# Kernel optimization log

Measured on AMD Instinct MI355X. Metric: run time of the kernel, lower is better.

The kernel has to match this reference:

```python
import jax, jax.numpy as jnp
import numpy as np

N = 50000
E = 800000
F_IN = 128
HID = 16
HEADS = 8
CLS = 16
NEG_SLOPE = 0.2


def setup_inputs() -> dict:
    key = jax.random.key(0)
    ks = jax.random.split(key, 12)
    x = jax.random.normal(ks[0], (N, F_IN), dtype=jnp.float32)
    edge_index = jax.random.randint(ks[1], (2, E), 0, N, dtype=jnp.int32)
    s = 0.1
    W1 = jax.random.normal(ks[2], (F_IN, HEADS * HID), dtype=jnp.float32) * s
    att_src1 = jax.random.normal(ks[3], (HEADS, HID), dtype=jnp.float32) * s
    att_dst1 = jax.random.normal(ks[4], (HEADS, HID), dtype=jnp.float32) * s
    b1 = jax.random.normal(ks[5], (HEADS * HID,), dtype=jnp.float32) * s
    W2 = jax.random.normal(ks[6], (HEADS * HID, CLS), dtype=jnp.float32) * s
    att_src2 = jax.random.normal(ks[7], (1, CLS), dtype=jnp.float32) * s
    att_dst2 = jax.random.normal(ks[8], (1, CLS), dtype=jnp.float32) * s
    b2 = jax.random.normal(ks[9], (CLS,), dtype=jnp.float32) * s
    return {"x": x, "edge_index": edge_index, "W1": W1, "att_src1": att_src1,
            "att_dst1": att_dst1, "b1": b1, "W2": W2, "att_src2": att_src2,
            "att_dst2": att_dst2, "b2": b2}


def _gat_conv(x, src, dst, W, a_src, a_dst, b, heads, out_ch, concat):
    n = x.shape[0]
    h = (x @ W).reshape(n, heads, out_ch)                     # [N,H,C]
    alpha_src = (h * a_src[None]).sum(-1)                     # [N,H]
    alpha_dst = (h * a_dst[None]).sum(-1)                     # [N,H]
    e = jax.nn.leaky_relu(alpha_src[src] + alpha_dst[dst], NEG_SLOPE)  # [E,H]
    m = jax.lax.stop_gradient(jax.ops.segment_max(e, dst, num_segments=n))
    e = jnp.exp(e - m[dst])
    denom = jax.ops.segment_sum(e, dst, num_segments=n)
    alpha = e / (denom[dst] + 1e-16)                          # [E,H]
    msg = h[src] * alpha[:, :, None]                          # [E,H,C]
    out = jax.ops.segment_sum(msg, dst, num_segments=n)       # [N,H,C]
    out = out.reshape(n, heads * out_ch) if concat else out.mean(axis=1)
    return out + b


def reference(x, edge_index, W1, att_src1, att_dst1, b1, W2, att_src2, att_dst2, b2):
    # PyG GATConv default add_self_loops=True
    loop = jnp.arange(N, dtype=edge_index.dtype)
    src = jnp.concatenate([edge_index[0], loop])
    dst = jnp.concatenate([edge_index[1], loop])
    h = _gat_conv(x, src, dst, W1, att_src1, att_dst1, b1, HEADS, HID, True)
    h = jax.nn.elu(h)
    # dropout inactive (eval mode)
    out = _gat_conv(h, src, dst, W2, att_src2, att_dst2, b2, 1, CLS, False)
    return out
```

## Files before the change

kernel.cpp:

```cpp
#include <hip/hip_runtime.h>
#include <hip/hip_bf16.h>
#include <limits.h>
#include <math.h>

#define N 50000
#define E_ 800000
#define ETOT 850000
#define HH 128
#define HEADS 8
#define HID 16
#define CLS 16
#define NEG 0.2f
#define NB ((N + 255) / 256)
#define GBM 64
#define GEMM_NB ((N + GBM - 1) / GBM)
#define LINK_NB ((ETOT + 255) / 256)
#define A1_NB ((N*HEADS + 255) / 256)

typedef unsigned short u16;
typedef unsigned int   u32;
typedef short s8v __attribute__((ext_vector_type(8)));
typedef float f4v __attribute__((ext_vector_type(4)));

__device__ __forceinline__ u16 f2bu(float f){
  union{float f; u32 i;} c; c.f = f;
  u32 lsb = (c.i >> 16) & 1u;
  c.i += 0x7fffu + lsb;
  return (u16)(c.i >> 16);
}
__device__ __forceinline__ float bu2f(u16 u){
  union{u32 i; float f;} c; c.i = ((u32)u) << 16; return c.f;
}
__device__ __forceinline__ float blo(u32 u){ union{u32 i; float f;} c; c.i = u << 16; return c.f; }
__device__ __forceinline__ float bhi(u32 u){ union{u32 i; float f;} c; c.i = u & 0xffff0000u; return c.f; }

__global__ __launch_bounds__(256) void k_prepW(const float* __restrict__ W,
                                               u16* __restrict__ wth, u16* __restrict__ wtl){
  int i = blockIdx.x*256 + threadIdx.x;
  if(i >= 128*128) return;
  int k = i >> 7, c = i & 127;
  float v = W[i];
  u16 hi = f2bu(v);
  u16 lo = f2bu(v - bu2f(hi));
  wth[c*128 + k] = hi;
  wtl[c*128 + k] = lo;
}

__global__ __launch_bounds__(256) void k_gemm1link(const float* __restrict__ x,
                                                   const u16* __restrict__ wth,
                                                   const u16* __restrict__ wtl,
                                                   u16* __restrict__ h1b,
                                                   const int* __restrict__ ei,
                                                   int* __restrict__ head,
                                                   int* __restrict__ srcv,
                                                   int* __restrict__ nxt){
  __shared__ u16 xh[GBM][40], xl[GBM][40];
  __shared__ u16 wh[128][40], wl[128][40];
  if(blockIdx.x >= GEMM_NB){
    int e = (blockIdx.x - GEMM_NB)*256 + threadIdx.x;
    if(e < ETOT){
      int s, d;
      if(e < E_){ s = ei[e]; d = ei[E_ + e]; } else { s = d = e - E_; }
      int old = atomicExch(&head[d], e);
      srcv[e] = s;
      nxt[e]  = old;
    }
    return;
  }
  int tid  = threadIdx.x;
  int wv   = tid >> 6;
  int lane = tid & 63;
  int row0 = blockIdx.x * GBM;

  f4v acc[4][2];
  #pragma unroll
  for(int t=0;t<4;t++)
    #pragma unroll
    for(int u=0;u<2;u++) acc[t][u] = (f4v){0.f,0.f,0.f,0.f};

  int xr  = tid >> 2;
  int xkq = (tid & 3) * 8;
  int wc  = tid & 127;
  int wq  = (tid >> 7) * 8;
  int xrow = row0 + xr; if(xrow >= N) xrow = N-1;
  const float* xb = x + (size_t)xrow*128 + xkq;
  int fr = lane & 15, fg = lane >> 4;
  int kk = fg*8;

  for(int kc=0; kc<4; kc++){
    int k0 = kc*32;
    float4 v0 = *(const float4*)(xb + k0);
    float4 v1 = *(const float4*)(xb + k0 + 4);
    __syncthreads();
    {
      float vv[8] = {v0.x,v0.y,v0.z,v0.w,v1.x,v1.y,v1.z,v1.w};
      s8v H, L;
      #pragma unroll
      for(int j=0;j<8;j++){
        u16 h_ = f2bu(vv[j]);
        H[j] = (short)h_;
        L[j] = (short)f2bu(vv[j] - bu2f(h_));
      }
      *(s8v*)&xh[xr][xkq] = H;
      *(s8v*)&xl[xr][xkq] = L;
    }
    #pragma unroll
    for(int j=0;j<2;j++){
      int kq = wq + j*16;
      *(s8v*)&wh[wc][kq] = *(const s8v*)&wth[wc*128 + k0 + kq];
      *(s8v*)&wl[wc][kq] = *(const s8v*)&wtl[wc*128 + k0 + kq];
    }
    __syncthreads();
    s8v a_h[4], a_l[4], b_h[2], b_l[2];
    #pragma unroll
    for(int t=0;t<4;t++){
      a_h[t] = *(const s8v*)&xh[t*16 + fr][kk];
      a_l[t] = *(const s8v*)&xl[t*16 + fr][kk];
    }
    #pragma unroll
    for(int u=0;u<2;u++){
      int col = wv*32 + u*16 + fr;
      b_h[u] = *(const s8v*)&wh[col][kk];
      b_l[u] = *(const s8v*)&wl[col][kk];
    }
    #pragma unroll
    for(int t=0;t<4;t++){
      #pragma unroll
      for(int u=0;u<2;u++){
        acc[t][u] = __builtin_amdgcn_mfma_f32_16x16x32_bf16(a_h[t], b_h[u], acc[t][u], 0,0,0);
        acc[t][u] = __builtin_amdgcn_mfma_f32_16x16x32_bf16(a_h[t], b_l[u], acc[t][u], 0,0,0);
        acc[t][u] = __builtin_amdgcn_mfma_f32_16x16x32_bf16(a_l[t], b_h[u], acc[t][u], 0,0,0);
      }
    }
  }
  #pragma unroll
  for(int t=0;t<4;t++){
    #pragma unroll
    for(int j=0;j<4;j++){
      int row = row0 + t*16 + fg*4 + j;
      if(row < N){
        u16* dst = h1b + (size_t)row*128 + wv*32 + fr;
        dst[0]  = f2bu(acc[t][0][j]);
        dst[16] = f2bu(acc[t][1][j]);
      }
    }
  }
}

__global__ __launch_bounds__(256) void k_alphascan1(const u16* __restrict__ h1b,
                                                    const float* __restrict__ Asv,
                                                    const float* __restrict__ Adv,
                                                    float* __restrict__ as1,
                                                    float* __restrict__ ad1,
                                                    const int* __restrict__ head,
                                                    const int* __restrict__ nxt,
                                                    int* __restrict__ deg,
                                                    int* __restrict__ bsum){
  __shared__ int sm[256];
  if(blockIdx.x < NB){
    int t = threadIdx.x;
    int i = blockIdx.x*256 + t;
    int cnt = 0;
    if(i < N){
      int e = head[i];
      while(e >= 0){ cnt++; e = nxt[e]; }
      deg[i] = cnt;
    }
    sm[t] = cnt;
    __syncthreads();
    #pragma unroll
    for(int ofs=128; ofs>0; ofs>>=1){
      if(t < ofs) sm[t] += sm[t+ofs];
      __syncthreads();
    }
    if(t == 0) bsum[blockIdx.x] = sm[0];
    return;
  }
  int id = (blockIdx.x - NB)*256 + threadIdx.x;
  if(id >= N*HEADS) return;
  int i = id >> 3, h = id & 7;
  const uint4* hv = (const uint4*)(h1b + (size_t)i*HH + h*HID);
  uint4 u0 = hv[0], u1 = hv[1];
  float vals[16] = {blo(u0.x),bhi(u0.x),blo(u0.y),bhi(u0.y),
                    blo(u0.z),bhi(u0.z),blo(u0.w),bhi(u0.w),
                    blo(u1.x),bhi(u1.x),blo(u1.y),bhi(u1.y),
                    blo(u1.z),bhi(u1.z),blo(u1.w),bhi(u1.w)};
  float s=0.f, d=0.f;
  #pragma unroll
  for(int j=0;j<16;j++){
    s = fmaf(vals[j], Asv[h*HID+j], s);
    d = fmaf(vals[j], Adv[h*HID+j], d);
  }
  as1[id]=s; ad1[id]=d;
}

__global__ __launch_bounds__(256) void k_scan3walk(const int* __restrict__ deg,
                                                   const int* __restrict__ bsum,
                                                   const int* __restrict__ head,
                                                   const int* __restrict__ srcv,
                                                   const int* __restrict__ nxt,
                                                   int* __restrict__ off,
                                                   int* __restrict__ csr){
  __shared__ int red[256];
  __shared__ int sm[256];
  int t = threadIdx.x;
  red[t] = (t < blockIdx.x) ? bsum[t] : 0;
  __syncthreads();
  #pragma unroll
  for(int ofs=128; ofs>0; ofs>>=1){
    if(t < ofs) red[t] += red[t+ofs];
    __syncthreads();
  }
  int boff = red[0];
  int i = blockIdx.x*256 + t;
  int v0 = (i < N) ? deg[i] : 0;
  sm[t] = v0;
  __syncthreads();
  #pragma unroll
  for(int ofs=1; ofs<256; ofs<<=1){
    int v = sm[t];
    int add = (t >= ofs) ? sm[t-ofs] : 0;
    __syncthreads();
    sm[t] = v + add;
    __syncthreads();
  }
  if(i < N){
    int excl = boff + sm[t] - v0;
    off[i] = excl;
    if(i == N-1) off[N] = excl + v0;
    int e = head[i];
    int pos = excl;
    while(e >= 0){
      csr[pos++] = srcv[e];
      e = nxt[e];
    }
  }
}

#define CH 64
__global__ __launch_bounds__(256) void k_agg1(const int* __restrict__ off,
                                              const int* __restrict__ csr,
                                              const float* __restrict__ as1,
                                              const float* __restrict__ ad1,
                                              const u32* __restrict__ h1w,
                                              const float* __restrict__ b1,
                                              u32* __restrict__ helu_w){
  __shared__ float wsm[4][CH*8];
  __shared__ int   ssm[4][CH];
  int wv   = threadIdx.x >> 6;
  int lane = threadIdx.x & 63;
  int node = blockIdx.x*4 + wv;
  int beg = off[node], end = off[node+1];
  int h  = lane >> 3;
  int hh = lane & 7;
  int el = lane >> 3;
  float advA = ad1[node*8 + hh];
  float den = 0.f, num0 = 0.f, num1 = 0.f;
  float* wsw = wsm[wv];
  int*   ssw = ssm[wv];
  const u32* hp = h1w + lane;
  for(int base = beg; base < end; base += CH){
    int cnt = end - base; if(cnt > CH) cnt = CH;
    #pragma unroll
    for(int k=0;k<CH;k+=8){
      int e = el + k;
      if(e < cnt){
        int s = csr[base+e];
        if(hh == 0) ssw[e] = s;
        float v = as1[s*8+hh] + advA;
        v = v > 0.f ? v : NEG*v;
        wsw[e*8+hh] = __expf(v);
      }
    }
    int e = 0;
    for(; e+8 <= cnt; e += 8){
      int ss[8]; float ww[8]; u32 uu[8];
      #pragma unroll
      for(int j=0;j<8;j++){ ss[j] = ssw[e+j]; ww[j] = wsw[(e+j)*8+h]; }
      #pragma unroll
      for(int j=0;j<8;j++){ uu[j] = hp[(size_t)ss[j]*64]; }
      #pragma unroll
      for(int j=0;j<8;j++){
        den += ww[j];
        num0 = fmaf(ww[j], blo(uu[j]), num0);
        num1 = fmaf(ww[j], bhi(uu[j]), num1);
      }
    }
    for(; e < cnt; e++){
      int s = ssw[e];
      float w = wsw[e*8+h];
      u32 u = hp[(size_t)s*64];
      den += w;
      num0 = fmaf(w, blo(u), num0);
      num1 = fmaf(w, bhi(u), num1);
    }
  }
  float2 bb = ((const float2*)b1)[lane];
  float inv = 1.f / (den + 1e-16f);
  float r0 = num0*inv + bb.x;
  float r1 = num1*inv + bb.y;
  r0 = r0 > 0.f ? r0 : expm1f(r0);
  r1 = r1 > 0.f ? r1 : expm1f(r1);
  helu_w[(size_t)node*64 + lane] = (u32)f2bu(r0) | ((u32)f2bu(r1) << 16);
}

__global__ __launch_bounds__(256) void k_gemm2(const u16* __restrict__ hb,
                                               const float* __restrict__ W2,
                                               const float* __restrict__ Asv,
                                               const float* __restrict__ Adv,
                                               u16* __restrict__ h2b,
                                               float* __restrict__ as2,
                                               float* __restrict__ ad2){
  __shared__ float Wl[128*16];
  int tid = threadIdx.x;
  const float4* W4 = (const float4*)W2;
  float4* Wl4 = (float4*)Wl;
  Wl4[tid]       = W4[tid];
  Wl4[tid + 256] = W4[tid + 256];
  __syncthreads();
  int i = blockIdx.x*16 + (tid >> 4);
  int c = tid & 15;
  if(i >= N) return;
  const uint4* h8 = (const uint4*)(hb + (size_t)i*HH);
  float acc = 0.f;
  #pragma unroll
  for(int ch=0; ch<16; ch++){
    uint4 u = h8[ch];
    int k = ch*8;
    acc = fmaf(blo(u.x), Wl[(k+0)*16+c], acc);
    acc = fmaf(bhi(u.x), Wl[(k+1)*16+c], acc);
    acc = fmaf(blo(u.y), Wl[(k+2)*16+c], acc);
    acc = fmaf(bhi(u.y), Wl[(k+3)*16+c], acc);
    acc = fmaf(blo(u.z), Wl[(k+4)*16+c], acc);
    acc = fmaf(bhi(u.z), Wl[(k+5)*16+c], acc);
    acc = fmaf(blo(u.w), Wl[(k+6)*16+c], acc);
    acc = fmaf(bhi(u.w), Wl[(k+7)*16+c], acc);
  }
  h2b[(size_t)i*CLS + c] = f2bu(acc);
  float ps = acc * Asv[c];
  float pd = acc * Adv[c];
  ps += __shfl_xor(ps,1); ps += __shfl_xor(ps,2); ps += __shfl_xor(ps,4); ps += __shfl_xor(ps,8);
  pd += __shfl_xor(pd,1); pd += __shfl_xor(pd,2); pd += __shfl_xor(pd,4); pd += __shfl_xor(pd,8);
  if(c == 0){ as2[i] = ps; ad2[i] = pd; }
}

__global__ __launch_bounds__(256) void k_agg2(const int* __restrict__ off,
                                              const int* __restrict__ csr,
                                              const float* __restrict__ as2,
                                              const float* __restrict__ ad2,
                                              const u32* __restrict__ h2w,
                                              const float* __restrict__ b2,
                                              float* __restrict__ outp){
  int t = threadIdx.x;
  int node = blockIdx.x*32 + (t >> 3);
  int c2 = t & 7;
  if(node >= N) return;
  int beg = off[node], end = off[node+1];
  float adv = ad2[node];
  float den = 0.f, num0 = 0.f, num1 = 0.f;
  for(int base = beg; base < end; base += 8){
    int cnt = end - base; if(cnt > 8) cnt = 8;
    float w_my = 0.f; int s_my = 0;
    if(c2 < cnt){
      s_my = csr[base + c2];
      float v = as2[s_my] + adv;
      v = v > 0.f ? v : NEG*v;
      w_my = __expf(v);
    }
    #pragma unroll
    for(int j=0; j<8; j++){
      if(j >= cnt) break;
      int src = (t & 56) | j;
      float w = __shfl(w_my, src);
      int   s = __shfl(s_my, src);
      u32 u = h2w[(size_t)s*8 + c2];
      den += w;
      num0 = fmaf(w, blo(u), num0);
      num1 = fmaf(w, bhi(u), num1);
    }
  }
  float inv = 1.f / (den + 1e-16f);
  float2 bb = ((const float2*)b2)[c2];
  float2 r;
  r.x = num0*inv + bb.x;
  r.y = num1*inv + bb.y;
  ((float2*)outp)[(size_t)node*8 + c2] = r;
}

extern "C" void kernel_launch(void* const* d_in, const int* in_sizes, int n_in,
                              void* d_out, int out_size, void* d_ws, size_t ws_size,
                              hipStream_t stream){
  const float* x     = (const float*)d_in[0];
  const int*   ei    = (const int*)  d_in[1];
  const float* W1    = (const float*)d_in[2];
  const float* av_s1 = (const float*)d_in[3];
  const float* av_d1 = (const float*)d_in[4];
  const float* b1    = (const float*)d_in[5];
  const float* W2    = (const float*)d_in[6];
  const float* av_s2 = (const float*)d_in[7];
  const float* av_d2 = (const float*)d_in[8];
  const float* b2    = (const float*)d_in[9];
  float* outp = (float*)d_out;

  char* p = (char*)d_ws;
  auto alloc = [&](size_t bytes){ char* q = p; p += (bytes + 255) & ~(size_t)255; return q; };
  u16*   h1b    = (u16*)  alloc((size_t)N*HH*2);
  u16*   helu_b = (u16*)  alloc((size_t)N*HH*2);
  u16*   h2b    = (u16*)  alloc((size_t)N*CLS*2);
  float* as1    = (float*)alloc((size_t)N*HEADS*4);
  float* ad1    = (float*)alloc((size_t)N*HEADS*4);
  float* as2    = (float*)alloc((size_t)N*4);
  float* ad2    = (float*)alloc((size_t)N*4);
  int*   deg    = (int*)  alloc((size_t)N*4);
  int*   head   = (int*)  alloc((size_t)N*4);
  int*   off    = (int*)  alloc((size_t)(N+1)*4);
  int*   csr    = (int*)  alloc((size_t)ETOT*4);
  int*   srcv   = (int*)  alloc((size_t)ETOT*4);
  int*   nxt    = (int*)  alloc((size_t)ETOT*4);
  u16*   wth    = (u16*)  alloc((size_t)128*128*2);
  u16*   wtl    = (u16*)  alloc((size_t)128*128*2);
  int*   bsum   = (int*)  alloc((size_t)NB*4);

  hipMemsetAsync(head, 0xFF, (size_t)N*4, stream);

  k_prepW<<<(128*128+255)/256, 256, 0, stream>>>(W1, wth, wtl);

  k_gemm1link<<<GEMM_NB + LINK_NB, 256, 0, stream>>>(x, wth, wtl, h1b, ei, head, srcv, nxt);

  k_alphascan1<<<NB + A1_NB, 256, 0, stream>>>(h1b, av_s1, av_d1, as1, ad1, head, nxt, deg, bsum);

  k_scan3walk<<<NB, 256, 0, stream>>>(deg, bsum, head, srcv, nxt, off, csr);

  k_agg1<<<N/4, 256, 0, stream>>>(off, csr, as1, ad1, (const u32*)h1b, b1, (u32*)helu_b);

  k_gemm2<<<(N+15)/16, 256, 0, stream>>>(helu_b, W2, av_s2, av_d2, h2b, as2, ad2);
  k_agg2<<<(N+31)/32, 256, 0, stream>>>(off, csr, as2, ad2, (const u32*)h2b, b2, outp);
}
```

Before: 160.4 us.

## Use MFMA for layer-2 GEMM, batch gathers in aggregation kernels, shrink agg1 chunk

Replaces the scalar FMA layer-2 GEMM with a bf16 MFMA kernel that uses split hi/lo W2 weights prepared alongside W1 in a merged prep kernel. Separately, agg1's edge chunk shrinks from 64 to 32 and gains a 4-wide unrolled gather tail, and agg2's gather loop is restructured to issue all 8 loads before accumulating. The aim is more memory-level parallelism in the gathers and less ALU time in gemm2, at the cost of extra workspace and a bf16 split approximation of W2.

```diff
diff --git a/kernel.cpp b/kernel.cpp
--- a/kernel.cpp
+++ b/kernel.cpp
@@ -34,16 +34,25 @@
 __device__ __forceinline__ float blo(u32 u){ union{u32 i; float f;} c; c.i = u << 16; return c.f; }
 __device__ __forceinline__ float bhi(u32 u){ union{u32 i; float f;} c; c.i = u & 0xffff0000u; return c.f; }
 
-__global__ __launch_bounds__(256) void k_prepW(const float* __restrict__ W,
-                                               u16* __restrict__ wth, u16* __restrict__ wtl){
+__global__ __launch_bounds__(256) void k_prep(const float* __restrict__ W1,
+                                              const float* __restrict__ W2,
+                                              u16* __restrict__ wth, u16* __restrict__ wtl,
+                                              u16* __restrict__ w2th, u16* __restrict__ w2tl){
   int i = blockIdx.x*256 + threadIdx.x;
-  if(i >= 128*128) return;
-  int k = i >> 7, c = i & 127;
-  float v = W[i];
-  u16 hi = f2bu(v);
-  u16 lo = f2bu(v - bu2f(hi));
-  wth[c*128 + k] = hi;
-  wtl[c*128 + k] = lo;
+  if(i < 128*128){
+    int k = i >> 7, c = i & 127;
+    float v = W1[i];
+    u16 hi = f2bu(v);
+    wth[c*128 + k] = hi;
+    wtl[c*128 + k] = f2bu(v - bu2f(hi));
+  }
+  if(i < 128*16){
+    int k = i >> 4, c = i & 15;
+    float v = W2[i];
+    u16 hi = f2bu(v);
+    w2th[c*128 + k] = hi;
+    w2tl[c*128 + k] = f2bu(v - bu2f(hi));
+  }
 }
 
 __global__ __launch_bounds__(256) void k_gemm1link(const float* __restrict__ x,
@@ -237,7 +246,7 @@
   }
 }
 
-#define CH 64
+#define CH 32
 __global__ __launch_bounds__(256) void k_agg1(const int* __restrict__ off,
                                               const int* __restrict__ csr,
                                               const float* __restrict__ as1,
@@ -286,6 +295,19 @@
         num1 = fmaf(ww[j], bhi(uu[j]), num1);
       }
     }
+    for(; e+4 <= cnt; e += 4){
+      int ss[4]; float ww[4]; u32 uu[4];
+      #pragma unroll
+      for(int j=0;j<4;j++){ ss[j] = ssw[e+j]; ww[j] = wsw[(e+j)*8+h]; }
+      #pragma unroll
+      for(int j=0;j<4;j++){ uu[j] = hp[(size_t)ss[j]*64]; }
+      #pragma unroll
+      for(int j=0;j<4;j++){
+        den += ww[j];
+        num0 = fmaf(ww[j], blo(uu[j]), num0);
+        num1 = fmaf(ww[j], bhi(uu[j]), num1);
+      }
+    }
     for(; e < cnt; e++){
       int s = ssw[e];
       float w = wsw[e*8+h];
@@ -304,44 +326,57 @@
   helu_w[(size_t)node*64 + lane] = (u32)f2bu(r0) | ((u32)f2bu(r1) << 16);
 }
 
-__global__ __launch_bounds__(256) void k_gemm2(const u16* __restrict__ hb,
-                                               const float* __restrict__ W2,
-                                               const float* __restrict__ Asv,
-                                               const float* __restrict__ Adv,
-                                               u16* __restrict__ h2b,
-                                               float* __restrict__ as2,
-                                               float* __restrict__ ad2){
-  __shared__ float Wl[128*16];
-  int tid = threadIdx.x;
-  const float4* W4 = (const float4*)W2;
-  float4* Wl4 = (float4*)Wl;
-  Wl4[tid]       = W4[tid];
-  Wl4[tid + 256] = W4[tid + 256];
+__global__ __launch_bounds__(256) void k_gemm2m(const u16* __restrict__ helu,
+                                                const u16* __restrict__ w2th,
+                                                const u16* __restrict__ w2tl,
+                                                const float* __restrict__ Asv,
+                                                const float* __restrict__ Adv,
+                                                u16* __restrict__ h2b,
+                                                float* __restrict__ as2,
+                                                float* __restrict__ ad2){
+  __shared__ u16 At[4][16][136];
+  __shared__ u16 Bh[16][136], Bl[16][136];
+  int tid  = threadIdx.x;
+  int wv   = tid >> 6;
+  int lane = tid & 63;
+  int fr = lane & 15, fg = lane >> 4;
+  int row0 = blockIdx.x*64 + wv*16;
+
+  {
+    int r = tid >> 4, c8 = (tid & 15)*8;
+    *(s8v*)&Bh[r][c8] = *(const s8v*)&w2th[r*128 + c8];
+    *(s8v*)&Bl[r][c8] = *(const s8v*)&w2tl[r*128 + c8];
+  }
+  #pragma unroll
+  for(int j=0;j<4;j++){
+    int rl = j*4 + (lane >> 4);
+    int rg = row0 + rl; if(rg >= N) rg = N-1;
+    *(s8v*)&At[wv][rl][(lane & 15)*8] = *(const s8v*)&helu[(size_t)rg*128 + (lane & 15)*8];
+  }
   __syncthreads();
-  int i = blockIdx.x*16 + (tid >> 4);
-  int c = tid & 15;
-  if(i >= N) return;
-  const uint4* h8 = (const uint4*)(hb + (size_t)i*HH);
-  float acc = 0.f;
-  #pragma unroll
-  for(int ch=0; ch<16; ch++){
-    uint4 u = h8[ch];
-    int k = ch*8;
-    acc = fmaf(blo(u.x), Wl[(k+0)*16+c], acc);
-    acc = fmaf(bhi(u.x), Wl[(k+1)*16+c], acc);
-    acc = fmaf(blo(u.y), Wl[(k+2)*16+c], acc);
-    acc = fmaf(bhi(u.y), Wl[(k+3)*16+c], acc);
-    acc = fmaf(blo(u.z), Wl[(k+4)*16+c], acc);
-    acc = fmaf(bhi(u.z), Wl[(k+5)*16+c], acc);
-    acc = fmaf(blo(u.w), Wl[(k+6)*16+c], acc);
-    acc = fmaf(bhi(u.w), Wl[(k+7)*16+c], acc);
-  }
-  h2b[(size_t)i*CLS + c] = f2bu(acc);
-  float ps = acc * Asv[c];
-  float pd = acc * Adv[c];
-  ps += __shfl_xor(ps,1); ps += __shfl_xor(ps,2); ps += __shfl_xor(ps,4); ps += __shfl_xor(ps,8);
-  pd += __shfl_xor(pd,1); pd += __shfl_xor(pd,2); pd += __shfl_xor(pd,4); pd += __shfl_xor(pd,8);
-  if(c == 0){ as2[i] = ps; ad2[i] = pd; }
+
+  f4v acc = (f4v){0.f,0.f,0.f,0.f};
+  #pragma unroll
+  for(int kc=0; kc<4; kc++){
+    int kk = kc*32 + fg*8;
+    s8v a  = *(const s8v*)&At[wv][fr][kk];
+    s8v bh = *(const s8v*)&Bh[fr][kk];
+    s8v bl = *(const s8v*)&Bl[fr][kk];
+    acc = __builtin_amdgcn_mfma_f32_16x16x32_bf16(a, bh, acc, 0,0,0);
+    acc = __builtin_amdgcn_mfma_f32_16x16x32_bf16(a, bl, acc, 0,0,0);
+  }
+  float asv = Asv[fr], adv = Adv[fr];
+  #pragma unroll
+  for(int j=0;j<4;j++){
+    int row = row0 + fg*4 + j;
+    float ps = acc[j]*asv, pd = acc[j]*adv;
+    ps += __shfl_xor(ps,1); ps += __shfl_xor(ps,2); ps += __shfl_xor(ps,4); ps += __shfl_xor(ps,8);
+    pd += __shfl_xor(pd,1); pd += __shfl_xor(pd,2); pd += __shfl_xor(pd,4); pd += __shfl_xor(pd,8);
+    if(row < N){
+      h2b[(size_t)row*16 + fr] = f2bu(acc[j]);
+      if(fr == 0){ as2[row] = ps; ad2[row] = pd; }
+    }
+  }
 }
 
 __global__ __launch_bounds__(256) void k_agg2(const int* __restrict__ off,
@@ -358,6 +393,7 @@
   int beg = off[node], end = off[node+1];
   float adv = ad2[node];
   float den = 0.f, num0 = 0.f, num1 = 0.f;
+  int gbase = t & 56;
   for(int base = beg; base < end; base += 8){
     int cnt = end - base; if(cnt > 8) cnt = 8;
     float w_my = 0.f; int s_my = 0;
@@ -367,16 +403,23 @@
       v = v > 0.f ? v : NEG*v;
       w_my = __expf(v);
     }
-    #pragma unroll
-    for(int j=0; j<8; j++){
-      if(j >= cnt) break;
-      int src = (t & 56) | j;
-      float w = __shfl(w_my, src);
-      int   s = __shfl(s_my, src);
-      u32 u = h2w[(size_t)s*8 + c2];
-      den += w;
-      num0 = fmaf(w, blo(u), num0);
-      num1 = fmaf(w, bhi(u), num1);
+    float ww[8]; int ss[8]; u32 uu[8];
+    #pragma unroll
+    for(int j=0;j<8;j++){
+      ww[j] = __shfl(w_my, gbase | j);
+      ss[j] = __shfl(s_my, gbase | j);
+    }
+    #pragma unroll
+    for(int j=0;j<8;j++){
+      if(j < cnt) uu[j] = h2w[(size_t)ss[j]*8 + c2];
+    }
+    #pragma unroll
+    for(int j=0;j<8;j++){
+      if(j < cnt){
+        den += ww[j];
+        num0 = fmaf(ww[j], blo(uu[j]), num0);
+        num1 = fmaf(ww[j], bhi(uu[j]), num1);
+      }
     }
   }
   float inv = 1.f / (den + 1e-16f);
@@ -419,11 +462,13 @@
   int*   nxt    = (int*)  alloc((size_t)ETOT*4);
   u16*   wth    = (u16*)  alloc((size_t)128*128*2);
   u16*   wtl    = (u16*)  alloc((size_t)128*128*2);
+  u16*   w2th   = (u16*)  alloc((size_t)16*128*2);
+  u16*   w2tl   = (u16*)  alloc((size_t)16*128*2);
   int*   bsum   = (int*)  alloc((size_t)NB*4);
 
   hipMemsetAsync(head, 0xFF, (size_t)N*4, stream);
 
-  k_prepW<<<(128*128+255)/256, 256, 0, stream>>>(W1, wth, wtl);
+  k_prep<<<(128*128+255)/256, 256, 0, stream>>>(W1, W2, wth, wtl, w2th, w2tl);
 
   k_gemm1link<<<GEMM_NB + LINK_NB, 256, 0, stream>>>(x, wth, wtl, h1b, ei, head, srcv, nxt);
 
@@ -433,6 +478,6 @@
 
   k_agg1<<<N/4, 256, 0, stream>>>(off, csr, as1, ad1, (const u32*)h1b, b1, (u32*)helu_b);
 
-  k_gemm2<<<(N+15)/16, 256, 0, stream>>>(helu_b, W2, av_s2, av_d2, h2b, as2, ad2);
+  k_gemm2m<<<(N+63)/64, 256, 0, stream>>>(helu_b, w2th, w2tl, av_s2, av_d2, h2b, as2, ad2);
   k_agg2<<<(N+31)/32, 256, 0, stream>>>(off, csr, as2, ad2, (const u32*)h2b, b2, outp);
 }
```

After: 147.8 us. 7.8% less time.
